# Optimization experiments

Hardware: AMD Instinct MI355X
Metric: run time of the kernel (lower is better)

Reference implementation:

```python
import jax, jax.numpy as jnp
import numpy as np

NEG_SLOPE = 0.2


def gat_conv(x, src, dst, n, W, a_src, a_dst, b):
    # x: [N, Din], W: [Din, Dout], a_src/a_dst: [Dout], b: [Dout]
    h = x @ W                                   # [N, Dout]
    alpha_src = h @ a_src                       # [N] score contribution of source nodes
    alpha_dst = h @ a_dst                       # [N]
    e = jax.nn.leaky_relu(alpha_src[src] + alpha_dst[dst], NEG_SLOPE)  # [E]
    # segment softmax over destination nodes (every node has a self-loop -> no empty segs)
    m = jax.ops.segment_max(e, dst, num_segments=n)
    p = jnp.exp(e - m[dst])
    denom = jax.ops.segment_sum(p, dst, num_segments=n)
    coeff = p / denom[dst]                      # [E]
    out = jax.ops.segment_sum(h[src] * coeff[:, None], dst, num_segments=n)
    return out + b


def setup_inputs() -> dict:
    key = jax.random.key(0)
    ks = jax.random.split(key, 16)
    N, E, D_IN, D_H, C = 50000, 800000, 256, 256, 10
    x = jax.random.normal(ks[0], (N, D_IN), dtype=jnp.float32)
    edge_index = jax.random.randint(ks[1], (2, E), 0, N, dtype=jnp.int64)
    s = 0.1
    params = {
        "W1": jax.random.normal(ks[2], (D_IN, D_H), jnp.float32) * s,
        "a_src1": jax.random.normal(ks[3], (D_H,), jnp.float32) * s,
        "a_dst1": jax.random.normal(ks[4], (D_H,), jnp.float32) * s,
        "b1": jnp.zeros((D_H,), jnp.float32),
        "W2": jax.random.normal(ks[5], (D_H, D_H), jnp.float32) * s,
        "a_src2": jax.random.normal(ks[6], (D_H,), jnp.float32) * s,
        "a_dst2": jax.random.normal(ks[7], (D_H,), jnp.float32) * s,
        "b2": jnp.zeros((D_H,), jnp.float32),
        "W3": jax.random.normal(ks[8], (D_H, C), jnp.float32) * s,
        "a_src3": jax.random.normal(ks[9], (C,), jnp.float32) * s,
        "a_dst3": jax.random.normal(ks[10], (C,), jnp.float32) * s,
        "b3": jnp.zeros((C,), jnp.float32),
    }
    return {"x": x, "edge_index": edge_index, **params}


def reference(x, edge_index, W1, a_src1, a_dst1, b1, W2, a_src2, a_dst2, b2,
              W3, a_src3, a_dst3, b3):
    n = x.shape[0]
    # PyG GATConv default add_self_loops=True
    loops = jnp.arange(n, dtype=edge_index.dtype)
    src = jnp.concatenate([edge_index[0], loops])
    dst = jnp.concatenate([edge_index[1], loops])
    h = gat_conv(x, src, dst, n, W1, a_src1, a_dst1, b1)
    h = jax.nn.relu(h)
    h = gat_conv(h, src, dst, n, W2, a_src2, a_dst2, b2)
    h = jax.nn.relu(h)
    out = gat_conv(h, src, dst, n, W3, a_src3, a_dst3, b3)
    return out
```

## Files before the change

kernel.cpp:

```cpp
#include <hip/hip_runtime.h>
#include <math.h>

#define N_NODES 50000
#define N_EDGES 800000
#define EP (N_EDGES + N_NODES)
#define NEG_SLOPE 0.2f
#define SCAN_BLOCKS ((N_NODES + 255) / 256)

typedef short short8 __attribute__((ext_vector_type(8)));
typedef float float4_ __attribute__((ext_vector_type(4)));

__device__ __forceinline__ unsigned short f2bf(float f) {
  unsigned int u = __float_as_uint(f);
  u = (u + 0x7FFFu + ((u >> 16) & 1u)) >> 16;
  return (unsigned short)u;
}
__device__ __forceinline__ float bf2f(unsigned int us) {
  return __uint_as_float(us << 16);
}


__global__ void cvt_wf_kernel(const float* __restrict__ W, unsigned short* __restrict__ Wf) {
  int t = blockIdx.x * 256 + threadIdx.x;
  int f = t >> 6, lane = t & 63;
  int nt = f >> 3, k0t = f & 7;
  int lm = lane & 15, kg = lane >> 4;
  int kbase = k0t * 32 + kg * 8;
  int n = nt * 16 + lm;
  short8 v;
#pragma unroll
  for (int j = 0; j < 8; ++j) v[j] = (short)f2bf(W[(size_t)(kbase + j) * 256 + n]);
  ((short8*)Wf)[t] = v;
}

__global__ void cvt_wf3_kernel(const float* __restrict__ W3, unsigned short* __restrict__ Wf3) {
  int t = blockIdx.x * 256 + threadIdx.x;
  int k0t = t >> 6, lane = t & 63;
  int lm = lane & 15, kg = lane >> 4;
  int kbase = k0t * 32 + kg * 8;
  short8 v;
#pragma unroll
  for (int j = 0; j < 8; ++j)
    v[j] = (lm < 10) ? (short)f2bf(W3[(size_t)(kbase + j) * 10 + lm]) : (short)0;
  ((short8*)Wf3)[t] = v;
}


__global__ void count_kernel(const int* __restrict__ ei, int* __restrict__ cnt) {
  int e = blockIdx.x * 256 + threadIdx.x;
  if (e >= EP) return;
  int dst = (e < N_EDGES) ? ei[N_EDGES + e] : (e - N_EDGES);
  atomicAdd(&cnt[dst], 1);
}

__global__ void scan1_kernel(const int* __restrict__ cnt, int* __restrict__ off,
                             int* __restrict__ bsum) {
  int i = blockIdx.x * 256 + threadIdx.x;
  int v = (i < N_NODES) ? cnt[i] : 0;
  int lane = threadIdx.x & 63, w = threadIdx.x >> 6;
  int x = v;
  for (int o = 1; o < 64; o <<= 1) { int y = __shfl_up(x, o); if (lane >= o) x += y; }
  __shared__ int wsum[4];
  if (lane == 63) wsum[w] = x;
  __syncthreads();
  int add = 0;
  for (int k = 0; k < w; ++k) add += wsum[k];
  if (i < N_NODES) off[i] = x - v + add;
  if (threadIdx.x == 255) bsum[blockIdx.x] = add + x;
}

__global__ void scan2_kernel(int* __restrict__ bsum, int* __restrict__ bpre,
                             int* __restrict__ off) {
  int t = threadIdx.x;
  int v = (t < SCAN_BLOCKS) ? bsum[t] : 0;
  int lane = t & 63, w = t >> 6;
  int x = v;
  for (int o = 1; o < 64; o <<= 1) { int y = __shfl_up(x, o); if (lane >= o) x += y; }
  __shared__ int wsum[4];
  if (lane == 63) wsum[w] = x;
  __syncthreads();
  int add = 0;
  for (int k = 0; k < w; ++k) add += wsum[k];
  if (t < SCAN_BLOCKS) bpre[t] = x - v + add;
  if (t == 255) off[N_NODES] = add + x;
}

__global__ void scan3_kernel(int* __restrict__ off, const int* __restrict__ bpre) {
  int i = blockIdx.x * 256 + threadIdx.x;
  if (i < N_NODES) off[i] += bpre[blockIdx.x];
}

__global__ void scatter_kernel(const int* __restrict__ ei, const int* __restrict__ off,
                               int* __restrict__ cnt, int* __restrict__ esrc) {
  int e = blockIdx.x * 256 + threadIdx.x;
  if (e >= EP) return;
  int src, dst;
  if (e < N_EDGES) { src = ei[e]; dst = ei[N_EDGES + e]; }
  else { src = dst = e - N_EDGES; }
  int pos = off[dst] + atomicAdd(&cnt[dst], 1);
  esrc[pos] = src;
}


template <int AF32>
__global__ __launch_bounds__(256, 1) void gemm_mfma3(const void* __restrict__ Av,
                                                     const uint4* __restrict__ Wf,
                                                     unsigned short* __restrict__ C,
                                                     const float* __restrict__ asrc,
                                                     const float* __restrict__ adst,
                                                     float* __restrict__ as_,
                                                     float* __restrict__ ad_, int M) {
  __shared__ uint4 Bl[8192];
  int tid = threadIdx.x;
#pragma unroll
  for (int i = 0; i < 32; ++i) Bl[i * 256 + tid] = Wf[i * 256 + tid];
  int wave = tid >> 6, lane = tid & 63;
  int lm = lane & 15, kg = lane >> 4;
  int row0 = blockIdx.x * 128 + wave * 32;
  int ar0 = row0 + lm, ar1 = row0 + 16 + lm;
  if (ar0 >= M) ar0 = M - 1;
  if (ar1 >= M) ar1 = M - 1;
  float4_ acc0[16], acc1[16];
#pragma unroll
  for (int i = 0; i < 16; ++i) { acc0[i] = (float4_){0, 0, 0, 0}; acc1[i] = (float4_){0, 0, 0, 0}; }
  __syncthreads();
  const short8* Bf = (const short8*)Bl;
  for (int k0t = 0; k0t < 8; ++k0t) {
    int k0 = k0t * 32;
    short8 a0, a1;
    if (AF32) {
      const float* A = (const float*)Av;
      const float* p0 = A + (size_t)ar0 * 256 + kg * 8 + k0;
      const float* p1 = A + (size_t)ar1 * 256 + kg * 8 + k0;
      float4 f0 = *(const float4*)p0, f1 = *(const float4*)(p0 + 4);
      float4 g0 = *(const float4*)p1, g1 = *(const float4*)(p1 + 4);
      a0 = (short8){(short)f2bf(f0.x), (short)f2bf(f0.y), (short)f2bf(f0.z), (short)f2bf(f0.w),
                    (short)f2bf(f1.x), (short)f2bf(f1.y), (short)f2bf(f1.z), (short)f2bf(f1.w)};
      a1 = (short8){(short)f2bf(g0.x), (short)f2bf(g0.y), (short)f2bf(g0.z), (short)f2bf(g0.w),
                    (short)f2bf(g1.x), (short)f2bf(g1.y), (short)f2bf(g1.z), (short)f2bf(g1.w)};
    } else {
      const unsigned short* A = (const unsigned short*)Av;
      a0 = *(const short8*)(A + (size_t)ar0 * 256 + kg * 8 + k0);
      a1 = *(const short8*)(A + (size_t)ar1 * 256 + kg * 8 + k0);
    }
#pragma unroll
    for (int nt = 0; nt < 16; ++nt) {
      short8 b = Bf[(nt * 8 + k0t) * 64 + lane];
      acc0[nt] = __builtin_amdgcn_mfma_f32_16x16x32_bf16(a0, b, acc0[nt], 0, 0, 0);
      acc1[nt] = __builtin_amdgcn_mfma_f32_16x16x32_bf16(a1, b, acc1[nt], 0, 0, 0);
    }
  }
  float avs[16], avd[16];
#pragma unroll
  for (int nt = 0; nt < 16; ++nt) { avs[nt] = asrc[nt * 16 + lm]; avd[nt] = adst[nt * 16 + lm]; }
#pragma unroll
  for (int g = 0; g < 2; ++g) {
    int rbase = row0 + g * 16 + kg * 4;
#pragma unroll
    for (int i = 0; i < 4; ++i) {
      int r = rbase + i;
      float s = 0.f, dd = 0.f;
#pragma unroll
      for (int nt = 0; nt < 16; ++nt) {
        float v = g ? acc1[nt][i] : acc0[nt][i];
        if (r < M) C[(size_t)r * 256 + nt * 16 + lm] = f2bf(v);
        s += v * avs[nt];
        dd += v * avd[nt];
      }
#pragma unroll
      for (int o = 1; o < 16; o <<= 1) { s += __shfl_xor(s, o); dd += __shfl_xor(dd, o); }
      if (lm == 0 && r < M) { as_[r] = s; ad_[r] = dd; }
    }
  }
}


__global__ __launch_bounds__(256) void gemm_c3_kernel(const unsigned short* __restrict__ X,
                                                      const unsigned short* __restrict__ Wf3,
                                                      const float* __restrict__ asrc,
                                                      const float* __restrict__ adst,
                                                      float* __restrict__ h3,
                                                      float* __restrict__ as_,
                                                      float* __restrict__ ad_, int M) {
  int tid = threadIdx.x;
  int wave = tid >> 6, lane = tid & 63;
  int lm = lane & 15, kg = lane >> 4;
  int row0 = blockIdx.x * 128 + wave * 32;
  int ar0 = row0 + lm, ar1 = row0 + 16 + lm;
  if (ar0 >= M) ar0 = M - 1;
  if (ar1 >= M) ar1 = M - 1;
  short8 bf[8];
#pragma unroll
  for (int k0t = 0; k0t < 8; ++k0t) bf[k0t] = ((const short8*)Wf3)[k0t * 64 + lane];
  float4_ acc0 = (float4_){0, 0, 0, 0}, acc1 = (float4_){0, 0, 0, 0};
#pragma unroll
  for (int k0t = 0; k0t < 8; ++k0t) {
    int k0 = k0t * 32;
    short8 a0 = *(const short8*)(X + (size_t)ar0 * 256 + kg * 8 + k0);
    short8 a1 = *(const short8*)(X + (size_t)ar1 * 256 + kg * 8 + k0);
    acc0 = __builtin_amdgcn_mfma_f32_16x16x32_bf16(a0, bf[k0t], acc0, 0, 0, 0);
    acc1 = __builtin_amdgcn_mfma_f32_16x16x32_bf16(a1, bf[k0t], acc1, 0, 0, 0);
  }
  float avs = (lm < 10) ? asrc[lm] : 0.f;
  float avd = (lm < 10) ? adst[lm] : 0.f;
#pragma unroll
  for (int g = 0; g < 2; ++g) {
    int rbase = row0 + g * 16 + kg * 4;
#pragma unroll
    for (int i = 0; i < 4; ++i) {
      int r = rbase + i;
      float v = g ? acc1[i] : acc0[i];
      if (r < M && lm < 10) h3[(size_t)r * 10 + lm] = v;
      float s = v * avs, dd = v * avd;
#pragma unroll
      for (int o = 1; o < 16; o <<= 1) { s += __shfl_xor(s, o); dd += __shfl_xor(dd, o); }
      if (lm == 0 && r < M) { as_[r] = s; ad_[r] = dd; }
    }
  }
}


__global__ __launch_bounds__(256) void agg_fused_kernel(const int* __restrict__ off,
                                                        const int* __restrict__ esrc,
                                                        const float* __restrict__ as_,
                                                        const float* __restrict__ ad_,
                                                        const unsigned short* __restrict__ h,
                                                        const float* __restrict__ bias,
                                                        unsigned short* __restrict__ outg) {
  __shared__ int s_src[4][64];
  __shared__ float s_p[4][64];
  int wave = threadIdx.x >> 6, lane = threadIdx.x & 63;
  int d = blockIdx.x * 4 + wave;
  if (d >= N_NODES) return;
  int s0 = off[d], s1 = off[d + 1];
  float adv = ad_[d];
  const uint2* hp = (const uint2*)h;
  float a0 = 0.f, a1 = 0.f, a2 = 0.f, a3 = 0.f;
  float sum = 0.f;
  for (int base = s0; base < s1; base += 64) {
    int m = s1 - base; if (m > 64) m = 64;
    int sv = 0; float p = 0.f;
    if (lane < m) {
      sv = esrc[base + lane];
      float e = as_[sv] + adv;
      e = e > 0.f ? e : NEG_SLOPE * e;
      p = __expf(e);
    }
    s_src[wave][lane] = sv;
    s_p[wave][lane] = p;
    float ps = p;
    for (int o = 32; o; o >>= 1) ps += __shfl_xor(ps, o);
    sum += ps;
    int j = 0;
    for (; j + 8 <= m; j += 8) {
#pragma unroll
      for (int u = 0; u < 8; ++u) {
        int src = s_src[wave][j + u];
        float w = s_p[wave][j + u];
        uint2 pv = hp[(size_t)src * 64 + lane];
        a0 = fmaf(w, bf2f(pv.x & 0xffffu), a0);
        a1 = fmaf(w, bf2f(pv.x >> 16), a1);
        a2 = fmaf(w, bf2f(pv.y & 0xffffu), a2);
        a3 = fmaf(w, bf2f(pv.y >> 16), a3);
      }
    }
    for (; j < m; ++j) {
      int src = s_src[wave][j];
      float w = s_p[wave][j];
      uint2 pv = hp[(size_t)src * 64 + lane];
      a0 = fmaf(w, bf2f(pv.x & 0xffffu), a0);
      a1 = fmaf(w, bf2f(pv.x >> 16), a1);
      a2 = fmaf(w, bf2f(pv.y & 0xffffu), a2);
      a3 = fmaf(w, bf2f(pv.y >> 16), a3);
    }
  }
  float inv = 1.0f / sum;
  float4 b4 = ((const float4*)bias)[lane];
  float o0 = fmaxf(fmaf(a0, inv, b4.x), 0.f);
  float o1 = fmaxf(fmaf(a1, inv, b4.y), 0.f);
  float o2 = fmaxf(fmaf(a2, inv, b4.z), 0.f);
  float o3 = fmaxf(fmaf(a3, inv, b4.w), 0.f);
  uint2 ov;
  ov.x = (unsigned int)f2bf(o0) | ((unsigned int)f2bf(o1) << 16);
  ov.y = (unsigned int)f2bf(o2) | ((unsigned int)f2bf(o3) << 16);
  ((uint2*)outg)[(size_t)d * 64 + lane] = ov;
}


__global__ void coeff3_kernel(const int* __restrict__ off, const int* __restrict__ esrc,
                              const float* __restrict__ as_, const float* __restrict__ ad_,
                              float* __restrict__ coeff, float* __restrict__ dinv) {
  int gid = blockIdx.x * blockDim.x + threadIdx.x;
  int d = gid >> 6, lane = threadIdx.x & 63;
  if (d >= N_NODES) return;
  int s0 = off[d], s1 = off[d + 1];
  float adv = ad_[d];
  float sum = 0.f;
  for (int s = s0 + lane; s < s1; s += 64) {
    float e = as_[esrc[s]] + adv;
    e = e > 0.f ? e : NEG_SLOPE * e;
    float p = __expf(e);
    coeff[s] = p;
    sum += p;
  }
  for (int o = 32; o; o >>= 1) sum += __shfl_xor(sum, o);
  if (lane == 0) dinv[d] = 1.0f / sum;
}


__global__ void agg10_kernel(const int* __restrict__ off, const int* __restrict__ esrc,
                             const float* __restrict__ coeff, const float* __restrict__ dinv,
                             const float* __restrict__ h, const float* __restrict__ bias,
                             float* __restrict__ out) {
  int gid = blockIdx.x * blockDim.x + threadIdx.x;
  int wid = gid >> 6;
  int lane = threadIdx.x & 63;
  int sub = lane >> 4, c = lane & 15;
  int d = wid * 4 + sub;
  if (d >= N_NODES || c >= 10) return;
  int s0 = off[d], s1 = off[d + 1];
  float acc = 0.f;
  for (int s = s0; s < s1; ++s)
    acc = fmaf(coeff[s], h[(size_t)esrc[s] * 10 + c], acc);
  out[(size_t)d * 10 + c] = fmaf(acc, dinv[d], bias[c]);
}


extern "C" void kernel_launch(void* const* d_in, const int* in_sizes, int n_in,
                              void* d_out, int out_size, void* d_ws, size_t ws_size,
                              hipStream_t stream) {
  const float* x   = (const float*)d_in[0];
  const int*   ei  = (const int*)d_in[1];
  const float* W1  = (const float*)d_in[2];
  const float* as1 = (const float*)d_in[3];
  const float* ad1 = (const float*)d_in[4];
  const float* b1  = (const float*)d_in[5];
  const float* W2  = (const float*)d_in[6];
  const float* as2 = (const float*)d_in[7];
  const float* ad2 = (const float*)d_in[8];
  const float* b2  = (const float*)d_in[9];
  const float* W3  = (const float*)d_in[10];
  const float* as3 = (const float*)d_in[11];
  const float* ad3 = (const float*)d_in[12];
  const float* b3  = (const float*)d_in[13];
  float* out = (float*)d_out;

  char* ws = (char*)d_ws;
  size_t off_b = 0;
  auto alloc = [&](size_t bytes) -> char* {
    char* p = ws + off_b;
    off_b += (bytes + 255) & ~(size_t)255;
    return p;
  };
  unsigned short* hb   = (unsigned short*)alloc((size_t)N_NODES * 256 * 2);
  unsigned short* gb   = (unsigned short*)alloc((size_t)N_NODES * 256 * 2);
  unsigned short* Wf1  = (unsigned short*)alloc(256 * 256 * 2);
  unsigned short* Wf2  = (unsigned short*)alloc(256 * 256 * 2);
  unsigned short* Wf3  = (unsigned short*)alloc(8 * 64 * 8 * 2);
  float* h3    = (float*)alloc((size_t)N_NODES * 10 * 4);
  float* as_   = (float*)alloc((size_t)N_NODES * 4);
  float* ad_   = (float*)alloc((size_t)N_NODES * 4);
  float* dinv  = (float*)alloc((size_t)N_NODES * 4);
  int*   roff  = (int*)alloc((size_t)(N_NODES + 1) * 4);
  int*   cnt   = (int*)alloc((size_t)N_NODES * 4);
  int*   bsum  = (int*)alloc((size_t)SCAN_BLOCKS * 4);
  int*   bpre  = (int*)alloc((size_t)SCAN_BLOCKS * 4);
  int*   esrc  = (int*)alloc((size_t)EP * 4);
  float* coeff = (float*)alloc((size_t)EP * 4);

  cvt_wf_kernel<<<32, 256, 0, stream>>>(W1, Wf1);
  cvt_wf_kernel<<<32, 256, 0, stream>>>(W2, Wf2);
  cvt_wf3_kernel<<<2, 256, 0, stream>>>(W3, Wf3);

  hipMemsetAsync(cnt, 0, N_NODES * 4, stream);
  int eb = (EP + 255) / 256;
  count_kernel<<<eb, 256, 0, stream>>>(ei, cnt);
  scan1_kernel<<<SCAN_BLOCKS, 256, 0, stream>>>(cnt, roff, bsum);
  scan2_kernel<<<1, 256, 0, stream>>>(bsum, bpre, roff);
  scan3_kernel<<<SCAN_BLOCKS, 256, 0, stream>>>(roff, bpre);
  hipMemsetAsync(cnt, 0, N_NODES * 4, stream);
  scatter_kernel<<<eb, 256, 0, stream>>>(ei, roff, cnt, esrc);

  int gblocks = (N_NODES + 127) / 128;
  int ablocks = (N_NODES + 3) / 4;
  int wgrid = (N_NODES * 64 + 255) / 256;
  int wgrid4 = (N_NODES * 16 + 255) / 256;

  gemm_mfma3<1><<<gblocks, 256, 0, stream>>>(x, (const uint4*)Wf1, hb, as1, ad1, as_, ad_, N_NODES);
  agg_fused_kernel<<<ablocks, 256, 0, stream>>>(roff, esrc, as_, ad_, hb, b1, gb);
  gemm_mfma3<0><<<gblocks, 256, 0, stream>>>(gb, (const uint4*)Wf2, hb, as2, ad2, as_, ad_, N_NODES);
  agg_fused_kernel<<<ablocks, 256, 0, stream>>>(roff, esrc, as_, ad_, hb, b2, gb);
  gemm_c3_kernel<<<gblocks, 256, 0, stream>>>(gb, Wf3, as3, ad3, h3, as_, ad_, N_NODES);
  coeff3_kernel<<<wgrid, 256, 0, stream>>>(roff, esrc, as_, ad_, coeff, dinv);
  agg10_kernel<<<wgrid4, 256, 0, stream>>>(roff, esrc, coeff, dinv, h3, b3, out);
}
```

Before: 428.3 us.

## Permute hidden feature layout for vectorized stores, widen GEMM blocks, fuse layer-3 softmax

GEMM outputs are now stored in a permuted column order, so each lane writes 16 contiguous bf16 values as two 16-byte stores. The next layer's weights, the biases and W3 are permuted to match. The GEMM block grows to 512 threads covering 256 rows, and the aggregation kernel handles two edges per wave using 16-byte gathers with a half-wave reduction. The final layer's coefficient kernel is merged into the aggregation kernel, which removes the coeff/dinv buffers and one launch. In exchange it adds layout bookkeeping across kernels, and `if (d >= N_NODES)` is dropped in agg_fused. That check is safe only because N is divisible by 4.

```diff
diff --git a/kernel.cpp b/kernel.cpp
--- a/kernel.cpp
+++ b/kernel.cpp
@@ -18,8 +18,16 @@
 __device__ __forceinline__ float bf2f(unsigned int us) {
   return __uint_as_float(us << 16);
 }
-
-
+__device__ __forceinline__ unsigned int pack2(float lo, float hi) {
+  return (unsigned int)f2bf(lo) | ((unsigned int)f2bf(hi) << 16);
+}
+
+__device__ __forceinline__ int permc(int p) {
+  return ((p & 0xE) << 4) | ((p & 1) << 4) | (p >> 4);
+}
+
+
+template <int PERM>
 __global__ void cvt_wf_kernel(const float* __restrict__ W, unsigned short* __restrict__ Wf) {
   int t = blockIdx.x * 256 + threadIdx.x;
   int f = t >> 6, lane = t & 63;
@@ -29,7 +37,10 @@
   int n = nt * 16 + lm;
   short8 v;
 #pragma unroll
-  for (int j = 0; j < 8; ++j) v[j] = (short)f2bf(W[(size_t)(kbase + j) * 256 + n]);
+  for (int j = 0; j < 8; ++j) {
+    int k = PERM ? permc(kbase + j) : (kbase + j);
+    v[j] = (short)f2bf(W[(size_t)k * 256 + n]);
+  }
   ((short8*)Wf)[t] = v;
 }
 
@@ -40,9 +51,19 @@
   int kbase = k0t * 32 + kg * 8;
   short8 v;
 #pragma unroll
-  for (int j = 0; j < 8; ++j)
-    v[j] = (lm < 10) ? (short)f2bf(W3[(size_t)(kbase + j) * 10 + lm]) : (short)0;
+  for (int j = 0; j < 8; ++j) {
+    int k = permc(kbase + j);
+    v[j] = (lm < 10) ? (short)f2bf(W3[(size_t)k * 10 + lm]) : (short)0;
+  }
   ((short8*)Wf3)[t] = v;
+}
+
+__global__ void permute_bias_kernel(const float* __restrict__ b1, const float* __restrict__ b2,
+                                    float* __restrict__ pb1, float* __restrict__ pb2) {
+  int p = threadIdx.x;
+  int c = permc(p);
+  pb1[p] = b1[c];
+  pb2[p] = b2[c];
 }
 
 
@@ -103,7 +124,7 @@
 
 
 template <int AF32>
-__global__ __launch_bounds__(256, 1) void gemm_mfma3(const void* __restrict__ Av,
+__global__ __launch_bounds__(512, 2) void gemm_mfma4(const void* __restrict__ Av,
                                                      const uint4* __restrict__ Wf,
                                                      unsigned short* __restrict__ C,
                                                      const float* __restrict__ asrc,
@@ -113,10 +134,10 @@
   __shared__ uint4 Bl[8192];
   int tid = threadIdx.x;
 #pragma unroll
-  for (int i = 0; i < 32; ++i) Bl[i * 256 + tid] = Wf[i * 256 + tid];
+  for (int i = 0; i < 16; ++i) Bl[i * 512 + tid] = Wf[i * 512 + tid];
   int wave = tid >> 6, lane = tid & 63;
   int lm = lane & 15, kg = lane >> 4;
-  int row0 = blockIdx.x * 128 + wave * 32;
+  int row0 = blockIdx.x * 256 + wave * 32;
   int ar0 = row0 + lm, ar1 = row0 + 16 + lm;
   if (ar0 >= M) ar0 = M - 1;
   if (ar1 >= M) ar1 = M - 1;
@@ -160,12 +181,19 @@
     for (int i = 0; i < 4; ++i) {
       int r = rbase + i;
       float s = 0.f, dd = 0.f;
-#pragma unroll
-      for (int nt = 0; nt < 16; ++nt) {
-        float v = g ? acc1[nt][i] : acc0[nt][i];
-        if (r < M) C[(size_t)r * 256 + nt * 16 + lm] = f2bf(v);
-        s += v * avs[nt];
-        dd += v * avd[nt];
+      unsigned int u[8];
+#pragma unroll
+      for (int j = 0; j < 8; ++j) {
+        float vlo = g ? acc1[2 * j][i] : acc0[2 * j][i];
+        float vhi = g ? acc1[2 * j + 1][i] : acc0[2 * j + 1][i];
+        u[j] = pack2(vlo, vhi);
+        s += vlo * avs[2 * j] + vhi * avs[2 * j + 1];
+        dd += vlo * avd[2 * j] + vhi * avd[2 * j + 1];
+      }
+      if (r < M) {
+        uint4* cp = (uint4*)(C + (size_t)r * 256 + lm * 16);
+        cp[0] = (uint4){u[0], u[1], u[2], u[3]};
+        cp[1] = (uint4){u[4], u[5], u[6], u[7]};
       }
 #pragma unroll
       for (int o = 1; o < 16; o <<= 1) { s += __shfl_xor(s, o); dd += __shfl_xor(dd, o); }
@@ -225,17 +253,17 @@
                                                         const float* __restrict__ as_,
                                                         const float* __restrict__ ad_,
                                                         const unsigned short* __restrict__ h,
-                                                        const float* __restrict__ bias,
+                                                        const float* __restrict__ pbias,
                                                         unsigned short* __restrict__ outg) {
   __shared__ int s_src[4][64];
   __shared__ float s_p[4][64];
   int wave = threadIdx.x >> 6, lane = threadIdx.x & 63;
+  int pair = lane >> 5, cl = lane & 31;
   int d = blockIdx.x * 4 + wave;
-  if (d >= N_NODES) return;
   int s0 = off[d], s1 = off[d + 1];
   float adv = ad_[d];
-  const uint2* hp = (const uint2*)h;
-  float a0 = 0.f, a1 = 0.f, a2 = 0.f, a3 = 0.f;
+  const uint4* hp4 = (const uint4*)h;
+  float a0 = 0.f, a1 = 0.f, a2 = 0.f, a3 = 0.f, a4 = 0.f, a5 = 0.f, a6 = 0.f, a7 = 0.f;
   float sum = 0.f;
   for (int base = s0; base < s1; base += 64) {
     int m = s1 - base; if (m > 64) m = 64;
@@ -251,78 +279,86 @@
     float ps = p;
     for (int o = 32; o; o >>= 1) ps += __shfl_xor(ps, o);
     sum += ps;
+    int nb = (m + 1) >> 1;
     int j = 0;
-    for (; j + 8 <= m; j += 8) {
-#pragma unroll
-      for (int u = 0; u < 8; ++u) {
-        int src = s_src[wave][j + u];
-        float w = s_p[wave][j + u];
-        uint2 pv = hp[(size_t)src * 64 + lane];
-        a0 = fmaf(w, bf2f(pv.x & 0xffffu), a0);
-        a1 = fmaf(w, bf2f(pv.x >> 16), a1);
-        a2 = fmaf(w, bf2f(pv.y & 0xffffu), a2);
-        a3 = fmaf(w, bf2f(pv.y >> 16), a3);
+    for (; j + 4 <= nb; j += 4) {
+#pragma unroll
+      for (int u = 0; u < 4; ++u) {
+        int idx = (j + u) * 2 + pair;
+        int src = s_src[wave][idx];
+        float w = s_p[wave][idx];
+        uint4 pv = hp4[(size_t)src * 32 + cl];
+        a0 = fmaf(w, bf2f(pv.x & 0xffffu), a0); a1 = fmaf(w, bf2f(pv.x >> 16), a1);
+        a2 = fmaf(w, bf2f(pv.y & 0xffffu), a2); a3 = fmaf(w, bf2f(pv.y >> 16), a3);
+        a4 = fmaf(w, bf2f(pv.z & 0xffffu), a4); a5 = fmaf(w, bf2f(pv.z >> 16), a5);
+        a6 = fmaf(w, bf2f(pv.w & 0xffffu), a6); a7 = fmaf(w, bf2f(pv.w >> 16), a7);
       }
     }
-    for (; j < m; ++j) {
-      int src = s_src[wave][j];
-      float w = s_p[wave][j];
-      uint2 pv = hp[(size_t)src * 64 + lane];
-      a0 = fmaf(w, bf2f(pv.x & 0xffffu), a0);
-      a1 = fmaf(w, bf2f(pv.x >> 16), a1);
-      a2 = fmaf(w, bf2f(pv.y & 0xffffu), a2);
-      a3 = fmaf(w, bf2f(pv.y >> 16), a3);
-    }
-  }
-  float inv = 1.0f / sum;
-  float4 b4 = ((const float4*)bias)[lane];
-  float o0 = fmaxf(fmaf(a0, inv, b4.x), 0.f);
-  float o1 = fmaxf(fmaf(a1, inv, b4.y), 0.f);
-  float o2 = fmaxf(fmaf(a2, inv, b4.z), 0.f);
-  float o3 = fmaxf(fmaf(a3, inv, b4.w), 0.f);
-  uint2 ov;
-  ov.x = (unsigned int)f2bf(o0) | ((unsigned int)f2bf(o1) << 16);
-  ov.y = (unsigned int)f2bf(o2) | ((unsigned int)f2bf(o3) << 16);
-  ((uint2*)outg)[(size_t)d * 64 + lane] = ov;
-}
-
-
-__global__ void coeff3_kernel(const int* __restrict__ off, const int* __restrict__ esrc,
-                              const float* __restrict__ as_, const float* __restrict__ ad_,
-                              float* __restrict__ coeff, float* __restrict__ dinv) {
-  int gid = blockIdx.x * blockDim.x + threadIdx.x;
-  int d = gid >> 6, lane = threadIdx.x & 63;
+    for (; j < nb; ++j) {
+      int idx = j * 2 + pair;
+      int src = s_src[wave][idx];
+      float w = s_p[wave][idx];
+      uint4 pv = hp4[(size_t)src * 32 + cl];
+      a0 = fmaf(w, bf2f(pv.x & 0xffffu), a0); a1 = fmaf(w, bf2f(pv.x >> 16), a1);
+      a2 = fmaf(w, bf2f(pv.y & 0xffffu), a2); a3 = fmaf(w, bf2f(pv.y >> 16), a3);
+      a4 = fmaf(w, bf2f(pv.z & 0xffffu), a4); a5 = fmaf(w, bf2f(pv.z >> 16), a5);
+      a6 = fmaf(w, bf2f(pv.w & 0xffffu), a6); a7 = fmaf(w, bf2f(pv.w >> 16), a7);
+    }
+  }
+  a0 += __shfl_xor(a0, 32); a1 += __shfl_xor(a1, 32);
+  a2 += __shfl_xor(a2, 32); a3 += __shfl_xor(a3, 32);
+  a4 += __shfl_xor(a4, 32); a5 += __shfl_xor(a5, 32);
+  a6 += __shfl_xor(a6, 32); a7 += __shfl_xor(a7, 32);
+  if (pair == 0) {
+    float inv = 1.0f / sum;
+    float4 b0 = ((const float4*)pbias)[2 * cl];
+    float4 b1 = ((const float4*)pbias)[2 * cl + 1];
+    float o0 = fmaxf(fmaf(a0, inv, b0.x), 0.f);
+    float o1 = fmaxf(fmaf(a1, inv, b0.y), 0.f);
+    float o2 = fmaxf(fmaf(a2, inv, b0.z), 0.f);
+    float o3 = fmaxf(fmaf(a3, inv, b0.w), 0.f);
+    float o4 = fmaxf(fmaf(a4, inv, b1.x), 0.f);
+    float o5 = fmaxf(fmaf(a5, inv, b1.y), 0.f);
+    float o6 = fmaxf(fmaf(a6, inv, b1.z), 0.f);
+    float o7 = fmaxf(fmaf(a7, inv, b1.w), 0.f);
+    uint4 ov = (uint4){pack2(o0, o1), pack2(o2, o3), pack2(o4, o5), pack2(o6, o7)};
+    ((uint4*)outg)[(size_t)d * 32 + cl] = ov;
+  }
+}
+
+
+__global__ void agg10_fused_kernel(const int* __restrict__ off, const int* __restrict__ esrc,
+                                   const float* __restrict__ as_, const float* __restrict__ ad_,
+                                   const float* __restrict__ h, const float* __restrict__ bias,
+                                   float* __restrict__ out) {
+  int gid = blockIdx.x * 256 + threadIdx.x;
+  int wid = gid >> 6, lane = threadIdx.x & 63;
+  int g = lane >> 4, c = lane & 15;
+  int d = wid * 4 + g;
   if (d >= N_NODES) return;
   int s0 = off[d], s1 = off[d + 1];
   float adv = ad_[d];
-  float sum = 0.f;
-  for (int s = s0 + lane; s < s1; s += 64) {
-    float e = as_[esrc[s]] + adv;
-    e = e > 0.f ? e : NEG_SLOPE * e;
-    float p = __expf(e);
-    coeff[s] = p;
-    sum += p;
-  }
-  for (int o = 32; o; o >>= 1) sum += __shfl_xor(sum, o);
-  if (lane == 0) dinv[d] = 1.0f / sum;
-}
-
-
-__global__ void agg10_kernel(const int* __restrict__ off, const int* __restrict__ esrc,
-                             const float* __restrict__ coeff, const float* __restrict__ dinv,
-                             const float* __restrict__ h, const float* __restrict__ bias,
-                             float* __restrict__ out) {
-  int gid = blockIdx.x * blockDim.x + threadIdx.x;
-  int wid = gid >> 6;
-  int lane = threadIdx.x & 63;
-  int sub = lane >> 4, c = lane & 15;
-  int d = wid * 4 + sub;
-  if (d >= N_NODES || c >= 10) return;
-  int s0 = off[d], s1 = off[d + 1];
-  float acc = 0.f;
-  for (int s = s0; s < s1; ++s)
-    acc = fmaf(coeff[s], h[(size_t)esrc[s] * 10 + c], acc);
-  out[(size_t)d * 10 + c] = fmaf(acc, dinv[d], bias[c]);
+  float acc = 0.f, sum = 0.f;
+  int s = s0;
+  for (; s + 2 <= s1; s += 2) {
+    int i0 = esrc[s], i1 = esrc[s + 1];
+    float e0 = as_[i0] + adv; e0 = e0 > 0.f ? e0 : NEG_SLOPE * e0;
+    float e1 = as_[i1] + adv; e1 = e1 > 0.f ? e1 : NEG_SLOPE * e1;
+    float h0 = (c < 10) ? h[(size_t)i0 * 10 + c] : 0.f;
+    float h1 = (c < 10) ? h[(size_t)i1 * 10 + c] : 0.f;
+    float p0 = __expf(e0), p1 = __expf(e1);
+    acc = fmaf(p0, h0, acc);
+    acc = fmaf(p1, h1, acc);
+    sum += p0 + p1;
+  }
+  if (s < s1) {
+    int i0 = esrc[s];
+    float e0 = as_[i0] + adv; e0 = e0 > 0.f ? e0 : NEG_SLOPE * e0;
+    float p0 = __expf(e0);
+    if (c < 10) acc = fmaf(p0, h[(size_t)i0 * 10 + c], acc);
+    sum += p0;
+  }
+  if (c < 10) out[(size_t)d * 10 + c] = fmaf(acc, 1.0f / sum, bias[c]);
 }
 
 
@@ -357,20 +393,21 @@
   unsigned short* Wf1  = (unsigned short*)alloc(256 * 256 * 2);
   unsigned short* Wf2  = (unsigned short*)alloc(256 * 256 * 2);
   unsigned short* Wf3  = (unsigned short*)alloc(8 * 64 * 8 * 2);
+  float* pb1   = (float*)alloc(256 * 4);
+  float* pb2   = (float*)alloc(256 * 4);
   float* h3    = (float*)alloc((size_t)N_NODES * 10 * 4);
   float* as_   = (float*)alloc((size_t)N_NODES * 4);
   float* ad_   = (float*)alloc((size_t)N_NODES * 4);
-  float* dinv  = (float*)alloc((size_t)N_NODES * 4);
   int*   roff  = (int*)alloc((size_t)(N_NODES + 1) * 4);
   int*   cnt   = (int*)alloc((size_t)N_NODES * 4);
   int*   bsum  = (int*)alloc((size_t)SCAN_BLOCKS * 4);
   int*   bpre  = (int*)alloc((size_t)SCAN_BLOCKS * 4);
   int*   esrc  = (int*)alloc((size_t)EP * 4);
-  float* coeff = (float*)alloc((size_t)EP * 4);
-
-  cvt_wf_kernel<<<32, 256, 0, stream>>>(W1, Wf1);
-  cvt_wf_kernel<<<32, 256, 0, stream>>>(W2, Wf2);
+
+  cvt_wf_kernel<0><<<32, 256, 0, stream>>>(W1, Wf1);
+  cvt_wf_kernel<1><<<32, 256, 0, stream>>>(W2, Wf2);
   cvt_wf3_kernel<<<2, 256, 0, stream>>>(W3, Wf3);
+  permute_bias_kernel<<<1, 256, 0, stream>>>(b1, b2, pb1, pb2);
 
   hipMemsetAsync(cnt, 0, N_NODES * 4, stream);
   int eb = (EP + 255) / 256;
@@ -381,16 +418,15 @@
   hipMemsetAsync(cnt, 0, N_NODES * 4, stream);
   scatter_kernel<<<eb, 256, 0, stream>>>(ei, roff, cnt, esrc);
 
-  int gblocks = (N_NODES + 127) / 128;
+  int g4blocks = (N_NODES + 255) / 256;
+  int g3blocks = (N_NODES + 127) / 128;
   int ablocks = (N_NODES + 3) / 4;
-  int wgrid = (N_NODES * 64 + 255) / 256;
   int wgrid4 = (N_NODES * 16 + 255) / 256;
 
-  gemm_mfma3<1><<<gblocks, 256, 0, stream>>>(x, (const uint4*)Wf1, hb, as1, ad1, as_, ad_, N_NODES);
-  agg_fused_kernel<<<ablocks, 256, 0, stream>>>(roff, esrc, as_, ad_, hb, b1, gb);
-  gemm_mfma3<0><<<gblocks, 256, 0, stream>>>(gb, (const uint4*)Wf2, hb, as2, ad2, as_, ad_, N_NODES);
-  agg_fused_kernel<<<ablocks, 256, 0, stream>>>(roff, esrc, as_, ad_, hb, b2, gb);
-  gemm_c3_kernel<<<gblocks, 256, 0, stream>>>(gb, Wf3, as3, ad3, h3, as_, ad_, N_NODES);
-  coeff3_kernel<<<wgrid, 256, 0, stream>>>(roff, esrc, as_, ad_, coeff, dinv);
-  agg10_kernel<<<wgrid4, 256, 0, stream>>>(roff, esrc, coeff, dinv, h3, b3, out);
-}
+  gemm_mfma4<1><<<g4blocks, 512, 0, stream>>>(x, (const uint4*)Wf1, hb, as1, ad1, as_, ad_, N_NODES);
+  agg_fused_kernel<<<ablocks, 256, 0, stream>>>(roff, esrc, as_, ad_, hb, pb1, gb);
+  gemm_mfma4<0><<<g4blocks, 512, 0, stream>>>(gb, (const uint4*)Wf2, hb, as2, ad2, as_, ad_, N_NODES);
+  agg_fused_kernel<<<ablocks, 256, 0, stream>>>(roff, esrc, as_, ad_, hb, pb2, gb);
+  gemm_c3_kernel<<<g3blocks, 256, 0, stream>>>(gb, Wf3, as3, ad3, h3, as_, ad_, N_NODES);
+  agg10_fused_kernel<<<wgrid4, 256, 0, stream>>>(roff, esrc, as_, ad_, h3, b3, out);
+}
```

New measurement: 379.3 us. 11.4% less time.
